# Kernel tuning notes

Hardware: AMD Instinct MI355X
Metric: run time of the kernel (lower is better)

## Reference

```python
import jax, jax.numpy as jnp
import numpy as np

K = 10       # APPNP propagation steps (PyG default)
ALPHA = 0.1  # teleport probability (PyG default)

N_NODES = 50000
N_EDGES = 800000
IN_CH = 64
HID_CH = 2 * IN_CH
OUT_CH = 64


def _gcn_norm(edge_index, num_nodes):
    # add self loops, symmetric normalization D^-1/2 (A+I) D^-1/2
    loops = jnp.arange(num_nodes, dtype=edge_index.dtype)
    src = jnp.concatenate([edge_index[0], loops])
    dst = jnp.concatenate([edge_index[1], loops])
    deg = jax.ops.segment_sum(jnp.ones_like(dst, dtype=jnp.float32), dst,
                              num_segments=num_nodes)
    dinv = jax.lax.rsqrt(jnp.maximum(deg, 1.0))
    norm = dinv[src] * dinv[dst]
    return src, dst, norm


def _appnp_prop(h, src, dst, norm, num_nodes):
    z = h
    for _ in range(K):
        msg = z[src] * norm[:, None]                       # [E+N, C]
        agg = jax.ops.segment_sum(msg, dst, num_segments=num_nodes)
        z = (1.0 - ALPHA) * agg + ALPHA * h
    return z


def setup_inputs() -> dict:
    key = jax.random.key(0)
    k1, k2, k3, k4, k5 = jax.random.split(key, 5)
    x = jax.random.normal(k1, (N_NODES, IN_CH), dtype=jnp.float32)
    edge_index = jax.random.randint(k2, (2, N_EDGES), 0, N_NODES, dtype=jnp.int64)
    W3 = jax.random.normal(k3, (IN_CH, HID_CH), dtype=jnp.float32) / np.sqrt(IN_CH)
    b3 = jnp.zeros((HID_CH,), dtype=jnp.float32)
    W4 = jax.random.normal(k4, (HID_CH, OUT_CH), dtype=jnp.float32) / np.sqrt(HID_CH)
    b4 = jnp.zeros((OUT_CH,), dtype=jnp.float32)
    return {"x": x, "edge_index": edge_index, "W3": W3, "b3": b3,
            "W4": W4, "b4": b4}


def reference(x, edge_index, W3, b3, W4, b4):
    n = x.shape[0]
    src, dst, norm = _gcn_norm(edge_index, n)
    h1 = x @ W3 + b3                               # [N, 2*in]
    h1 = _appnp_prop(h1, src, dst, norm, n)
    h1 = jax.nn.relu(h1)
    h2 = h1 @ W4 + b4                              # [N, out]
    return _appnp_prop(h2, src, dst, norm, n)
```

## Files before the change

### kernel.cpp

```cpp
#include <hip/hip_runtime.h>

#define PROP_ALPHA 0.1f
#define PROP_KSTEPS 10

typedef _Float16 half_t;
typedef __attribute__((ext_vector_type(4))) _Float16 half4v;
typedef __attribute__((ext_vector_type(8))) _Float16 half8v;
typedef __attribute__((ext_vector_type(4))) float f32x4;


__global__ void hist_kernel(const int* __restrict__ dst, int* __restrict__ degI, int E) {
    int e = blockIdx.x * blockDim.x + threadIdx.x;
    if (e < E) atomicAdd(&degI[dst[e]], 1);
}

__global__ void dinvz_kernel(const int* __restrict__ degI, float* __restrict__ dinv,
                             float* __restrict__ vA, float* __restrict__ vB, int N) {
    int i = blockIdx.x * blockDim.x + threadIdx.x;
    if (i < N) {
        float d = (float)(degI[i] + 1);
        dinv[i] = rsqrtf(d);
    } else if (i == N) {
        dinv[N] = 0.0f;
        vA[N] = 0.0f;
        vB[N] = 0.0f;
    }
}

__global__ __launch_bounds__(256) void scan1_kernel(const int* __restrict__ degI,
                                                    int* __restrict__ rowptr,
                                                    int* __restrict__ blockSums, int N) {
    __shared__ int s[256];
    int t = threadIdx.x;
    int idx = blockIdx.x * 256 + t;
    s[t] = (idx < N) ? ((degI[idx] + 3) & ~3) : 0;
    __syncthreads();
    for (int off = 1; off < 256; off <<= 1) {
        int x = (t >= off) ? s[t - off] : 0;
        __syncthreads();
        s[t] += x;
        __syncthreads();
    }
    if (idx < N) rowptr[idx + 1] = s[t];
    if (t == 255) blockSums[blockIdx.x] = s[255];
    if (blockIdx.x == 0 && t == 0) rowptr[0] = 0;
}

__global__ __launch_bounds__(256) void scan2_kernel(int* __restrict__ blockSums, int nB) {
    __shared__ int s[256];
    int t = threadIdx.x;
    s[t] = (t < nB) ? blockSums[t] : 0;
    __syncthreads();
    for (int off = 1; off < 256; off <<= 1) {
        int x = (t >= off) ? s[t - off] : 0;
        __syncthreads();
        s[t] += x;
        __syncthreads();
    }
    if (t < nB) blockSums[t] = (t == 0) ? 0 : s[t - 1];
}

__global__ void scan3_kernel(int* __restrict__ rowptr, const int* __restrict__ blockSums,
                             int N) {
    int idx = blockIdx.x * 256 + threadIdx.x;
    if (idx < N) rowptr[idx + 1] += blockSums[blockIdx.x];
}

__global__ void fillu_kernel(unsigned int* __restrict__ p, unsigned int val, int n) {
    int i = blockIdx.x * blockDim.x + threadIdx.x;
    if (i < n) p[i] = val;
}

__global__ void scatter_kernel(const int* __restrict__ src, const int* __restrict__ dst,
                               const int* __restrict__ rowptr, int* __restrict__ rowctr,
                               unsigned short* __restrict__ edata, int E) {
    int e = blockIdx.x * blockDim.x + threadIdx.x;
    if (e < E) {
        int d = dst[e];
        int p = rowptr[d] + atomicAdd(&rowctr[d], 1);
        edata[p] = (unsigned short)src[e];
    }
}


__global__ void prep_kernel(const float* __restrict__ x, const float* __restrict__ dinv,
                            half_t* __restrict__ z16A, half_t* __restrict__ z16B,
                            half_t* __restrict__ ah16, int N) {
    int i = blockIdx.x * blockDim.x + threadIdx.x;
    int nvec = (N + 1) * 16;
    if (i >= nvec) return;
    int row = i >> 4;
    if (row < N) {
        float4 v = reinterpret_cast<const float4*>(x)[i];
        float di = dinv[row];
        half4v z;
        z.x = (half_t)(di * v.x); z.y = (half_t)(di * v.y);
        z.z = (half_t)(di * v.z); z.w = (half_t)(di * v.w);
        reinterpret_cast<half4v*>(z16A)[i] = z;
        half4v a;
        a.x = (half_t)(PROP_ALPHA * di * v.x); a.y = (half_t)(PROP_ALPHA * di * v.y);
        a.z = (half_t)(PROP_ALPHA * di * v.z); a.w = (half_t)(PROP_ALPHA * di * v.w);
        reinterpret_cast<half4v*>(ah16)[i] = a;
    } else {
        half4v zz = {(half_t)0.f, (half_t)0.f, (half_t)0.f, (half_t)0.f};
        reinterpret_cast<half4v*>(z16A)[i] = zz;
        reinterpret_cast<half4v*>(z16B)[i] = zz;
    }
}


__global__ __launch_bounds__(256) void mfmamlp_kernel(const half_t* __restrict__ zx,
                                                      const float* __restrict__ vw,
                                                      const float* __restrict__ dinv,
                                                      const float* __restrict__ W3,
                                                      const float* __restrict__ b3,
                                                      const float* __restrict__ W4,
                                                      const float* __restrict__ b4,
                                                      half_t* __restrict__ z16o,
                                                      half_t* __restrict__ ah16o,
                                                      int N) {
    __shared__ half_t W3T[128 * 72];
    __shared__ half_t W4T[64 * 136];
    __shared__ half_t h1s[4][16 * 136];
    __shared__ float vds[4][16];
    __shared__ float dds[4][16];

    int t = threadIdx.x;
    int wv = t >> 6, lane = t & 63;
    int ln16 = lane & 15, kg = lane >> 4;
    int r0w = blockIdx.x * 64 + wv * 16;

    for (int idx = t; idx < 64 * 128; idx += 256) {
        int k = idx >> 7, c = idx & 127;
        W3T[c * 72 + k] = (half_t)W3[idx];
    }
    for (int idx = t; idx < 128 * 64; idx += 256) {
        int k = idx >> 6, c = idx & 63;
        W4T[c * 136 + k] = (half_t)W4[idx];
    }
    if (lane < 16) {
        int r = r0w + lane;
        float di = (r < N) ? dinv[r] : 0.0f;
        dds[wv][lane] = di;
        vds[wv][lane] = (r < N && di > 0.0f) ? vw[r] / di : 0.0f;
    }
    __syncthreads();

    int rowg = r0w + ln16;
    int rowc = (rowg < N) ? rowg : N;
    float rds = (rowg < N) ? 1.0f / dinv[rowg] : 0.0f;
    half8v a1[2];
    #pragma unroll
    for (int h = 0; h < 2; ++h) {
        half8v w8 = *reinterpret_cast<const half8v*>(
            &zx[(size_t)rowc * 64 + h * 32 + kg * 8]);
        half8v s;
        #pragma unroll
        for (int j = 0; j < 8; ++j) s[j] = (half_t)((float)w8[j] * rds);
        a1[h] = s;
    }

    #pragma unroll
    for (int ct = 0; ct < 8; ++ct) {
        float b3c = b3[ct * 16 + ln16];
        f32x4 acc;
        #pragma unroll
        for (int r = 0; r < 4; ++r) acc[r] = vds[wv][kg * 4 + r] * b3c;
        const half_t* wbase = &W3T[(ct * 16 + ln16) * 72 + kg * 8];
        half8v b10 = *reinterpret_cast<const half8v*>(wbase);
        half8v b11 = *reinterpret_cast<const half8v*>(wbase + 32);
        acc = __builtin_amdgcn_mfma_f32_16x16x32_f16(a1[0], b10, acc, 0, 0, 0);
        acc = __builtin_amdgcn_mfma_f32_16x16x32_f16(a1[1], b11, acc, 0, 0, 0);
        #pragma unroll
        for (int r = 0; r < 4; ++r)
            h1s[wv][(kg * 4 + r) * 136 + ct * 16 + ln16] =
                (half_t)fmaxf(acc[r], 0.0f);
    }

    #pragma unroll
    for (int ct2 = 0; ct2 < 4; ++ct2) {
        float b4c = b4[ct2 * 16 + ln16];
        f32x4 acc = {b4c, b4c, b4c, b4c};
        #pragma unroll
        for (int kh = 0; kh < 4; ++kh) {
            half8v a2 = *reinterpret_cast<const half8v*>(
                &h1s[wv][ln16 * 136 + kh * 32 + kg * 8]);
            half8v b2 = *reinterpret_cast<const half8v*>(
                &W4T[(ct2 * 16 + ln16) * 136 + kh * 32 + kg * 8]);
            acc = __builtin_amdgcn_mfma_f32_16x16x32_f16(a2, b2, acc, 0, 0, 0);
        }
        #pragma unroll
        for (int r = 0; r < 4; ++r) {
            int row = kg * 4 + r;
            int gr = r0w + row;
            if (gr < N) {
                float di = dds[wv][row];
                float val = acc[r];
                size_t base = (size_t)gr * 64 + ct2 * 16 + ln16;
                z16o[base] = (half_t)(di * val);
                ah16o[base] = (half_t)(PROP_ALPHA * di * val);
            }
        }
    }
}


template <bool WITHV>
__global__ __launch_bounds__(256, 8) void prop_kernel(
        const half_t* __restrict__ zin, const half_t* __restrict__ ah16,
        const int* __restrict__ rowptr, const unsigned short* __restrict__ edata,
        const float* __restrict__ dinv,
        half_t* __restrict__ zout, float* __restrict__ outF,
        const float* __restrict__ vin, float* __restrict__ vout,
        int N, int lastOut) {
    const int t = threadIdx.x;
    const int grp = t >> 3;
    const int l8 = t & 7;
    const int c = l8 << 3;
    int node = blockIdx.x * 32 + grp;
    if (node >= N) return;

    int beg = rowptr[node];
    int end = rowptr[node + 1];
    size_t selfbase = (size_t)node * 64 + c;

    half8v wself = *reinterpret_cast<const half8v*>(&zin[selfbase]);
    half8v ahh = *reinterpret_cast<const half8v*>(&ah16[selfbase]);
    float di = dinv[node];

    float acc[8];
    #pragma unroll
    for (int j = 0; j < 8; ++j) acc[j] = (float)wself[j];
    float vacc = WITHV ? vin[node] : 0.0f;

    for (int e = beg; e < end; e += 4) {
        ushort4 ss = *reinterpret_cast<const ushort4*>(&edata[e]);
        half8v z0 = *reinterpret_cast<const half8v*>(&zin[(size_t)ss.x * 64 + c]);
        half8v z1 = *reinterpret_cast<const half8v*>(&zin[(size_t)ss.y * 64 + c]);
        half8v z2 = *reinterpret_cast<const half8v*>(&zin[(size_t)ss.z * 64 + c]);
        half8v z3 = *reinterpret_cast<const half8v*>(&zin[(size_t)ss.w * 64 + c]);
        if (WITHV)
            vacc += (vin[ss.x] + vin[ss.y]) + (vin[ss.z] + vin[ss.w]);
        #pragma unroll
        for (int j = 0; j < 8; ++j) {
            float p0 = (float)z0[j] + (float)z1[j];
            float p1 = (float)z2[j] + (float)z3[j];
            acc[j] += p0 + p1;
        }
    }

    const float om = 1.0f - PROP_ALPHA;
    float dd = di * di;
    if (!lastOut) {
        half8v o;
        #pragma unroll
        for (int j = 0; j < 8; ++j)
            o[j] = (half_t)(om * dd * acc[j] + (float)ahh[j]);
        *reinterpret_cast<half8v*>(&zout[selfbase]) = o;
    } else {
        float rd = 1.0f / di;
        float r[8];
        #pragma unroll
        for (int j = 0; j < 8; ++j)
            r[j] = om * di * acc[j] + (float)ahh[j] * rd;
        float4 o0 = {r[0], r[1], r[2], r[3]};
        float4 o1 = {r[4], r[5], r[6], r[7]};
        *reinterpret_cast<float4*>(&outF[selfbase]) = o0;
        *reinterpret_cast<float4*>(&outF[selfbase + 4]) = o1;
    }
    if (WITHV && l8 == 0)
        vout[node] = om * dd * vacc + PROP_ALPHA * di;
}


extern "C" void kernel_launch(void* const* d_in, const int* in_sizes, int n_in,
                              void* d_out, int out_size, void* d_ws, size_t ws_size,
                              hipStream_t stream) {
    const float* x  = (const float*)d_in[0];
    const int*   ei = (const int*)d_in[1];
    const float* W3 = (const float*)d_in[2];
    const float* b3 = (const float*)d_in[3];
    const float* W4 = (const float*)d_in[4];
    const float* b4 = (const float*)d_in[5];
    float* out = (float*)d_out;

    int N = in_sizes[0] / 64;
    int E = in_sizes[1] / 2;
    const int* srcA = ei;
    const int* dstA = ei + E;

    char* ws = (char*)d_ws;
    size_t off = 0;
    auto alloc = [&](size_t bytes) -> void* {
        void* p = ws + off;
        off = (off + bytes + 255) & ~(size_t)255;
        return p;
    };

    int nScanB = (N + 255) / 256;
    size_t slotsMax = (size_t)E + 4 * (size_t)N;

    int*    degI   = (int*)alloc((size_t)N * 4);
    int*    rowptr = (int*)alloc(((size_t)N + 1) * 4);
    int*    rowctr = (int*)alloc((size_t)N * 4);
    int*    bsums  = (int*)alloc((size_t)nScanB * 4);
    float*  dinv   = (float*)alloc(((size_t)N + 1) * 4);
    unsigned short* edata = (unsigned short*)alloc(slotsMax * 2 + 16);
    float*  vA     = (float*)alloc(((size_t)N + 1) * 4);
    float*  vB     = (float*)alloc(((size_t)N + 1) * 4);
    half_t* z16A   = (half_t*)alloc(((size_t)N + 1) * 64 * 2);
    half_t* z16B   = (half_t*)alloc(((size_t)N + 1) * 64 * 2);
    half_t* ah16   = (half_t*)alloc(((size_t)N + 1) * 64 * 2);

    hipMemsetAsync(degI, 0, (size_t)N * 4, stream);
    hipMemsetAsync(rowctr, 0, (size_t)N * 4, stream);

    int nFill = (int)((slotsMax + 1) / 2);
    unsigned int fillv = ((unsigned int)N << 16) | (unsigned int)N;
    fillu_kernel<<<(nFill + 255) / 256, 256, 0, stream>>>((unsigned int*)edata, fillv, nFill);
    hist_kernel<<<(E + 255) / 256, 256, 0, stream>>>(dstA, degI, E);
    dinvz_kernel<<<(N + 256) / 256, 256, 0, stream>>>(degI, dinv, vA, vB, N);
    scan1_kernel<<<nScanB, 256, 0, stream>>>(degI, rowptr, bsums, N);
    scan2_kernel<<<1, 256, 0, stream>>>(bsums, nScanB);
    scan3_kernel<<<nScanB, 256, 0, stream>>>(rowptr, bsums, N);
    scatter_kernel<<<(E + 255) / 256, 256, 0, stream>>>(srcA, dstA, rowptr, rowctr,
                                                        edata, E);

    int nvec = (N + 1) * 16;
    int propBlocks = (N + 31) / 32;

    prep_kernel<<<(nvec + 255) / 256, 256, 0, stream>>>(x, dinv, z16A, z16B, ah16, N);
    for (int s = 0; s < PROP_KSTEPS; ++s) {
        const half_t* zi = (s & 1) ? z16B : z16A;
        half_t*       zo = (s & 1) ? z16A : z16B;
        const float*  vi = (s == 0) ? dinv : ((s & 1) ? vA : vB);
        float*        vo = (s & 1) ? vB : vA;
        prop_kernel<true><<<propBlocks, 256, 0, stream>>>(
            zi, ah16, rowptr, edata, dinv, zo, nullptr, vi, vo, N, 0);
    }

    mfmamlp_kernel<<<(N + 63) / 64, 256, 0, stream>>>(z16A, vB, dinv, W3, b3, W4, b4,
                                                      z16B, ah16, N);

    for (int s = 0; s < PROP_KSTEPS; ++s) {
        const half_t* zi = (s & 1) ? z16A : z16B;
        half_t*       zo = (s & 1) ? z16B : z16A;
        int last = (s == PROP_KSTEPS - 1) ? 1 : 0;
        prop_kernel<false><<<propBlocks, 256, 0, stream>>>(
            zi, ah16, rowptr, edata, dinv, zo, out, nullptr, nullptr, N, last);
    }
}
```

Baseline: 517.1 us.

## Order propagation nodes by degree bucket to balance per-wave work

Adds a counting sort that groups nodes by padded neighbour count (in groups of four), producing a permutation array. The prop kernel now maps each 8-lane group to perm[gid], so nodes with similar degree share a wavefront. This is meant to cut divergence and idle lanes from uneven loop trip counts in the gather loop. The cost is three small preprocessing kernels, one extra indirection per node, and scattered, less coalesced self-row and output accesses because node order no longer follows memory order.

```diff
diff --git a/kernel.cpp b/kernel.cpp
--- a/kernel.cpp
+++ b/kernel.cpp
@@ -79,6 +79,40 @@
         int d = dst[e];
         int p = rowptr[d] + atomicAdd(&rowctr[d], 1);
         edata[p] = (unsigned short)src[e];
+    }
+}
+
+
+__global__ void deghist_kernel(const int* __restrict__ rowptr, int* __restrict__ h256,
+                               int N) {
+    int i = blockIdx.x * blockDim.x + threadIdx.x;
+    if (i < N) {
+        int it = (rowptr[i + 1] - rowptr[i]) >> 2;
+        atomicAdd(&h256[it > 255 ? 255 : it], 1);
+    }
+}
+
+__global__ __launch_bounds__(256) void degscan_kernel(int* __restrict__ h256) {
+    __shared__ int s[256];
+    int t = threadIdx.x;
+    s[t] = h256[t];
+    __syncthreads();
+    for (int off = 1; off < 256; off <<= 1) {
+        int x = (t >= off) ? s[t - off] : 0;
+        __syncthreads();
+        s[t] += x;
+        __syncthreads();
+    }
+    h256[t] = (t == 0) ? 0 : s[t - 1];
+}
+
+__global__ void permscat_kernel(const int* __restrict__ rowptr, int* __restrict__ h256,
+                                int* __restrict__ perm, int N) {
+    int i = blockIdx.x * blockDim.x + threadIdx.x;
+    if (i < N) {
+        int it = (rowptr[i + 1] - rowptr[i]) >> 2;
+        int p = atomicAdd(&h256[it > 255 ? 255 : it], 1);
+        perm[p] = i;
     }
 }
 
@@ -209,7 +243,7 @@
 __global__ __launch_bounds__(256, 8) void prop_kernel(
         const half_t* __restrict__ zin, const half_t* __restrict__ ah16,
         const int* __restrict__ rowptr, const unsigned short* __restrict__ edata,
-        const float* __restrict__ dinv,
+        const float* __restrict__ dinv, const int* __restrict__ perm,
         half_t* __restrict__ zout, float* __restrict__ outF,
         const float* __restrict__ vin, float* __restrict__ vout,
         int N, int lastOut) {
@@ -217,8 +251,9 @@
     const int grp = t >> 3;
     const int l8 = t & 7;
     const int c = l8 << 3;
-    int node = blockIdx.x * 32 + grp;
-    if (node >= N) return;
+    int gid = blockIdx.x * 32 + grp;
+    if (gid >= N) return;
+    int node = perm[gid];
 
     int beg = rowptr[node];
     int end = rowptr[node + 1];
@@ -304,6 +339,8 @@
     int*    rowptr = (int*)alloc(((size_t)N + 1) * 4);
     int*    rowctr = (int*)alloc((size_t)N * 4);
     int*    bsums  = (int*)alloc((size_t)nScanB * 4);
+    int*    h256   = (int*)alloc(256 * 4);
+    int*    perm   = (int*)alloc((size_t)N * 4);
     float*  dinv   = (float*)alloc(((size_t)N + 1) * 4);
     unsigned short* edata = (unsigned short*)alloc(slotsMax * 2 + 16);
     float*  vA     = (float*)alloc(((size_t)N + 1) * 4);
@@ -314,6 +351,7 @@
 
     hipMemsetAsync(degI, 0, (size_t)N * 4, stream);
     hipMemsetAsync(rowctr, 0, (size_t)N * 4, stream);
+    hipMemsetAsync(h256, 0, 256 * 4, stream);
 
     int nFill = (int)((slotsMax + 1) / 2);
     unsigned int fillv = ((unsigned int)N << 16) | (unsigned int)N;
@@ -325,6 +363,9 @@
     scan3_kernel<<<nScanB, 256, 0, stream>>>(rowptr, bsums, N);
     scatter_kernel<<<(E + 255) / 256, 256, 0, stream>>>(srcA, dstA, rowptr, rowctr,
                                                         edata, E);
+    deghist_kernel<<<nScanB, 256, 0, stream>>>(rowptr, h256, N);
+    degscan_kernel<<<1, 256, 0, stream>>>(h256);
+    permscat_kernel<<<nScanB, 256, 0, stream>>>(rowptr, h256, perm, N);
 
     int nvec = (N + 1) * 16;
     int propBlocks = (N + 31) / 32;
@@ -336,7 +377,7 @@
         const float*  vi = (s == 0) ? dinv : ((s & 1) ? vA : vB);
         float*        vo = (s & 1) ? vB : vA;
         prop_kernel<true><<<propBlocks, 256, 0, stream>>>(
-            zi, ah16, rowptr, edata, dinv, zo, nullptr, vi, vo, N, 0);
+            zi, ah16, rowptr, edata, dinv, perm, zo, nullptr, vi, vo, N, 0);
     }
 
     mfmamlp_kernel<<<(N + 63) / 64, 256, 0, stream>>>(z16A, vB, dinv, W3, b3, W4, b4,
@@ -347,6 +388,6 @@
         half_t*       zo = (s & 1) ? z16B : z16A;
         int last = (s == PROP_KSTEPS - 1) ? 1 : 0;
         prop_kernel<false><<<propBlocks, 256, 0, stream>>>(
-            zi, ah16, rowptr, edata, dinv, zo, out, nullptr, nullptr, N, last);
-    }
-}
+            zi, ah16, rowptr, edata, dinv, perm, zo, out, nullptr, nullptr, N, last);
+    }
+}
```

New measurement: 1.115 ms. +115.7%, slower.
